# Kernel optimization log

Measured on AMD Instinct MI355X. Metric: run time of the kernel, lower is better.

The kernel has to match this reference:

```python
import jax, jax.numpy as jnp
import numpy as np

B = 128          # batch of codewords
M_CHK = 288      # n_check_nodes
N_VAR = 576      # n_variable_nodes
K_INFO = 288     # n_information_bits
N_ITER = 5
EDGE_P = 0.02    # ~11-12 edges per check row, LDPC-like sparsity


def setup_inputs() -> dict:
    key = jax.random.key(0)
    k1, k2, k3, k4 = jax.random.split(key, 4)
    inputs = jax.random.normal(k1, (B, N_VAR), dtype=jnp.float32)
    # sparse binary parity-check matrix, batched (keras RNN constants carry batch dim)
    H = jax.random.bernoulli(k2, EDGE_P, (B, M_CHK, N_VAR)).astype(jnp.float32)
    sigma2 = 0.5 + 0.5 * jax.random.uniform(k3, (B, 1), dtype=jnp.float32)
    # learned parameters
    input_ponderation = jnp.ones((N_ITER, 1), dtype=jnp.float32)
    out_ponderation = jnp.ones((N_ITER, 1), dtype=jnp.float32)
    skip_ponderation = jnp.ones((1, 1), dtype=jnp.float32)
    # per-edge check-to-variable weights of the neural BP cell
    w_cv = 1.0 + 0.02 * jax.random.normal(k4, (M_CHK, N_VAR), dtype=jnp.float32)
    gate_logit = jnp.asarray(0.0, dtype=jnp.float32)
    return {"inputs": inputs, "H": H, "sigma2": sigma2,
            "input_ponderation": input_ponderation,
            "out_ponderation": out_ponderation,
            "skip_ponderation": skip_ponderation,
            "w_cv": w_cv, "gate_logit": gate_logit}


def _decode(inputs, H, sigma2, input_ponderation, out_ponderation,
            skip_ponderation, w_cv, gate_logit):
    llrs = -4.0 * inputs / sigma2                                    # [B, n]
    # trainable=True path: normalize by mean |llr|
    norm_llrs = llrs / jnp.mean(jnp.abs(llrs), axis=-1, keepdims=True)
    # tile over iterations and apply input ponderation -> [B, T, n]
    x = norm_llrs[:, None, :] * input_ponderation

    mask = H                                                         # [B, m, n]
    gate = jax.nn.sigmoid(gate_logit)

    def cell(Mstate, x_t):
        # variable-to-check extrinsic messages on edges
        S = jnp.sum(Mstate, axis=1, keepdims=True)                   # [B, 1, n]
        V = (x_t[:, None, :] + S - Mstate) * mask                    # [B, m, n]
        # tanh-product check-node update (product excluding self via divide)
        t = jnp.tanh(0.5 * jnp.clip(V, -15.0, 15.0))
        t_edge = jnp.where(mask > 0, t, 1.0)
        P = jnp.prod(t_edge, axis=-1, keepdims=True)                 # [B, m, 1]
        t_safe = jnp.where(jnp.abs(t_edge) < 1e-7,
                           jnp.where(t_edge >= 0, 1e-7, -1e-7), t_edge)
        r = jnp.clip(P / t_safe, -1.0 + 1e-6, 1.0 - 1e-6)
        M_new = 2.0 * jnp.arctanh(r) * w_cv * mask                   # weighted c2v
        # gated (damped) state update
        M_out = gate * M_new + (1.0 - gate) * Mstate
        posterior = x_t + jnp.sum(M_out, axis=1)                     # [B, n]
        return M_out, posterior

    M0 = jnp.zeros_like(H)
    xs = jnp.swapaxes(x, 0, 1)                                       # [T, B, n]
    _, posts = jax.lax.scan(cell, M0, xs)
    outputs = jnp.swapaxes(posts, 0, 1)                              # [B, T, n]

    # post-normalization per iteration, weighted pooling over iterations
    norm_out = outputs / jnp.mean(jnp.abs(outputs), axis=-1, keepdims=True)
    pooled = jnp.mean(out_ponderation * norm_out, axis=-2)           # [B, n]
    out = pooled + skip_ponderation * norm_llrs                      # [1,1] broadcast
    return jax.nn.sigmoid(-out[:, :K_INFO])


def reference(inputs, H, sigma2, input_ponderation, out_ponderation,
              skip_ponderation, w_cv, gate_logit):
    return _decode(inputs, H, sigma2, input_ponderation, out_ponderation,
                   skip_ponderation, w_cv, gate_logit)
```

## Files before the change

kernel.cpp:

```cpp
#include <hip/hip_runtime.h>

#define B_SZ  128
#define MCHK  288
#define NVAR  576
#define KINFO 288
#define NITER 5
#define ECAP  3712
#define TPB   1024

__global__ __launch_bounds__(TPB) void decode(
    const float* __restrict__ inp,   const float* __restrict__ H,
    const float* __restrict__ sigma2,const float* __restrict__ ipond,
    const float* __restrict__ opond, const float* __restrict__ skipp,
    const float* __restrict__ wcv,   const float* __restrict__ gatel,
    float* __restrict__ out)
{
    __shared__ float Mld[ECAP];
    __shared__ float tld[ECAP];
    __shared__ float wld[ECAP];
    __shared__ unsigned int ev[ECAP];
    __shared__ float Sb[NITER + 1][NVAR];
    __shared__ float xln[NVAR];
    __shared__ float Prow[MCHK];
    __shared__ int   rcnt[MCHK], roff[MCHK];
    __shared__ float red[NITER * 16];
    __shared__ float scalv[NITER];
    __shared__ int   Ecnt;

    const int b    = blockIdx.x;
    const int tid  = threadIdx.x;
    const int wid  = tid >> 6;
    const int lane = tid & 63;

    const float sig  = sigma2[b];
    const float gate = 1.0f / (1.0f + __expf(-gatel[0]));
    const float gbar = 1.0f - gate;

    float ipl[NITER], opl[NITER];
    #pragma unroll
    for (int t = 0; t < NITER; ++t) { ipl[t] = ipond[t]; opl[t] = opond[t]; }

    float l = 0.0f, al = 0.0f, xv = 0.0f;
    if (tid < NVAR) { l = -4.0f * inp[(size_t)b * NVAR + tid] / sig; al = fabsf(l); }
    #pragma unroll
    for (int o = 32; o; o >>= 1) al += __shfl_down(al, o, 64);
    if (lane == 0) red[wid] = al;
    if (tid == 0) Ecnt = 0;
    for (int i = tid; i < (NITER + 1) * NVAR; i += TPB) ((float*)Sb)[i] = 0.0f;
    __syncthreads();
    if (wid == 0) {
        float s = (lane < 16) ? red[lane] : 0.0f;
        s += __shfl_down(s, 8, 64); s += __shfl_down(s, 4, 64);
        s += __shfl_down(s, 2, 64); s += __shfl_down(s, 1, 64);
        if (lane == 0) scalv[0] = (float)NVAR / s;
    }
    __syncthreads();
    if (tid < NVAR) { xv = l * scalv[0]; xln[tid] = xv; }

    {
        const float* Hb = H + (size_t)b * MCHK * NVAR;
        const unsigned long long lt = (1ull << lane) - 1ull;
        for (int i = 0; i < MCHK / 16; ++i) {
            int r = wid + 16 * i;
            const float4* h4 = (const float4*)(Hb + (size_t)r * NVAR);
            const float4* w4 = (const float4*)(wcv + (size_t)r * NVAR);
            float4 a  = h4[lane];
            float4 b4 = h4[64 + lane];
            float  c  = ((const float*)h4)[512 + lane];
            float4 wa = w4[lane];
            float4 wb = w4[64 + lane];
            float  wc = ((const float*)w4)[512 + lane];
            unsigned long long mk[9];
            mk[0]=__ballot(a.x!=0.f);  mk[1]=__ballot(a.y!=0.f);
            mk[2]=__ballot(a.z!=0.f);  mk[3]=__ballot(a.w!=0.f);
            mk[4]=__ballot(b4.x!=0.f); mk[5]=__ballot(b4.y!=0.f);
            mk[6]=__ballot(b4.z!=0.f); mk[7]=__ballot(b4.w!=0.f);
            mk[8]=__ballot(c!=0.f);
            int tot = 0;
            #pragma unroll
            for (int k = 0; k < 9; ++k) tot += __popcll(mk[k]);
            int o0 = 0;
            if (lane == 0) o0 = atomicAdd(&Ecnt, tot);
            o0 = __shfl(o0, 0, 64);
            int cc = (o0 >= ECAP) ? 0 : ((o0 + tot > ECAP) ? (ECAP - o0) : tot);
            if (lane == 0) { roff[r] = o0; rcnt[r] = cc; }
            float wv[9] = {wa.x, wa.y, wa.z, wa.w, wb.x, wb.y, wb.z, wb.w, wc};
            int base = 0;
            #pragma unroll
            for (int k = 0; k < 9; ++k) {
                bool nz = (mk[k] >> lane) & 1ull;
                int col = (k < 4) ? (4 * lane + k)
                        : (k < 8) ? (256 + 4 * lane + (k - 4))
                                  : (512 + lane);
                if (nz) {
                    int p = base + __popcll(mk[k] & lt);
                    if (p < cc) {
                        int e = o0 + p;
                        ev[e]  = ((unsigned)r << 16) | (unsigned)col;
                        wld[e] = wv[k];
                        Mld[e] = 0.0f;
                    }
                }
                base += __popcll(mk[k]);
            }
        }
    }
    __syncthreads();
    const int E = (Ecnt > ECAP) ? ECAP : Ecnt;

    for (int t = 0; t < NITER; ++t) {
        const float pt = ipl[t];
        const float* St = Sb[t];
        float*       Sn = Sb[t + 1];

        for (int e = tid; e < E; e += TPB) {
            int v   = (int)(ev[e] & 0xFFFFu);
            float V = fmaf(pt, xln[v], St[v]) - Mld[e];
            V = fminf(15.0f, fmaxf(-15.0f, V));
            float ex = __expf(V);
            float te = (ex - 1.0f) * __builtin_amdgcn_rcpf(ex + 1.0f);
            float x  = 0.5f * V, x2 = x * x;
            float tp = x * fmaf(x2, fmaf(x2, fmaf(x2, -0.05396825f, 0.13333333f),
                                         -0.33333333f), 1.0f);
            tld[e] = (fabsf(V) < 0.5f) ? tp : te;
        }
        __syncthreads();

        if (tid < MCHK) {
            int o = roff[tid], oe = o + rcnt[tid];
            float p0 = 1.0f, p1 = 1.0f, p2 = 1.0f, p3 = 1.0f;
            int j = o;
            for (; j + 4 <= oe; j += 4) {
                float t0 = tld[j], t1 = tld[j + 1], t2 = tld[j + 2], t3 = tld[j + 3];
                p0 *= t0; p1 *= t1; p2 *= t2; p3 *= t3;
            }
            for (; j < oe; ++j) p0 *= tld[j];
            Prow[tid] = (p0 * p1) * (p2 * p3);
        }
        __syncthreads();

        for (int e = tid; e < E; e += TPB) {
            unsigned pk = ev[e];
            int v = (int)(pk & 0xFFFFu);
            int r = (int)(pk >> 16);
            float tj = tld[e];
            float ts = (fabsf(tj) < 1e-7f) ? ((tj >= 0.0f) ? 1e-7f : -1e-7f) : tj;
            float rr = Prow[r] * __builtin_amdgcn_rcpf(ts);
            rr = fminf(1.0f - 1e-6f, fmaxf(-1.0f + 1e-6f, rr));
            float Mn = __logf((1.0f + rr) * __builtin_amdgcn_rcpf(1.0f - rr)) * wld[e];
            float Mo = fmaf(gate, Mn, gbar * Mld[e]);
            Mld[e] = Mo;
            atomicAdd(&Sn[v], Mo);
        }
        __syncthreads();
    }

    float ap[NITER] = {0, 0, 0, 0, 0};
    if (tid < NVAR) {
        #pragma unroll
        for (int t = 0; t < NITER; ++t)
            ap[t] = fabsf(fmaf(ipl[t], xv, Sb[t + 1][tid]));
    }
    #pragma unroll
    for (int o = 32; o; o >>= 1) {
        #pragma unroll
        for (int t = 0; t < NITER; ++t) ap[t] += __shfl_down(ap[t], o, 64);
    }
    if (lane == 0) {
        #pragma unroll
        for (int t = 0; t < NITER; ++t) red[t * 16 + wid] = ap[t];
    }
    __syncthreads();
    if (wid == 0) {
        #pragma unroll
        for (int t = 0; t < NITER; ++t) {
            float s = (lane < 16) ? red[t * 16 + lane] : 0.0f;
            s += __shfl_down(s, 8, 64); s += __shfl_down(s, 4, 64);
            s += __shfl_down(s, 2, 64); s += __shfl_down(s, 1, 64);
            if (lane == 0) scalv[t] = (float)NVAR / s;
        }
    }
    __syncthreads();
    if (tid < KINFO) {
        float acc = 0.0f;
        #pragma unroll
        for (int t = 0; t < NITER; ++t)
            acc += opl[t] * fmaf(ipl[t], xv, Sb[t + 1][tid]) * scalv[t];
        float o = acc * (1.0f / NITER) + skipp[0] * xv;
        out[(size_t)b * KINFO + tid] = 1.0f / (1.0f + __expf(o));
    }
}

extern "C" void kernel_launch(void* const* d_in, const int* in_sizes, int n_in,
                              void* d_out, int out_size, void* d_ws, size_t ws_size,
                              hipStream_t stream) {
    const float* inp    = (const float*)d_in[0];
    const float* H      = (const float*)d_in[1];
    const float* sigma2 = (const float*)d_in[2];
    const float* ipond  = (const float*)d_in[3];
    const float* opond  = (const float*)d_in[4];
    const float* skipp  = (const float*)d_in[5];
    const float* wcv    = (const float*)d_in[6];
    const float* gatel  = (const float*)d_in[7];
    float* out = (float*)d_out;

    decode<<<B_SZ, TPB, 0, stream>>>(inp, H, sigma2, ipond, opond, skipp,
                                     wcv, gatel, out);
}
```

Measured before the change: 182.0 us.

## Build sparse edge list via flat H scan and per-row prefix scan

```diff
diff --git a/kernel.cpp b/kernel.cpp
--- a/kernel.cpp
+++ b/kernel.cpp
@@ -6,7 +6,10 @@
 #define KINFO 288
 #define NITER 5
 #define ECAP  3712
+#define CAP2  32
 #define TPB   1024
+#define NQ4   (MCHK * NVAR / 4)
+#define Q4ROW (NVAR / 4)
 
 __global__ __launch_bounds__(TPB) void decode(
     const float* __restrict__ inp,   const float* __restrict__ H,
@@ -23,9 +26,10 @@
     __shared__ float xln[NVAR];
     __shared__ float Prow[MCHK];
     __shared__ int   rcnt[MCHK], roff[MCHK];
+    __shared__ unsigned short vpad[MCHK * CAP2];
     __shared__ float red[NITER * 16];
     __shared__ float scalv[NITER];
-    __shared__ int   Ecnt;
+    __shared__ int   wtot[8], wbase[8];
 
     const int b    = blockIdx.x;
     const int tid  = threadIdx.x;
@@ -45,7 +49,7 @@
     #pragma unroll
     for (int o = 32; o; o >>= 1) al += __shfl_down(al, o, 64);
     if (lane == 0) red[wid] = al;
-    if (tid == 0) Ecnt = 0;
+    if (tid < MCHK) rcnt[tid] = 0;
     for (int i = tid; i < (NITER + 1) * NVAR; i += TPB) ((float*)Sb)[i] = 0.0f;
     __syncthreads();
     if (wid == 0) {
@@ -58,55 +62,65 @@
     if (tid < NVAR) { xv = l * scalv[0]; xln[tid] = xv; }
 
     {
-        const float* Hb = H + (size_t)b * MCHK * NVAR;
-        const unsigned long long lt = (1ull << lane) - 1ull;
-        for (int i = 0; i < MCHK / 16; ++i) {
-            int r = wid + 16 * i;
-            const float4* h4 = (const float4*)(Hb + (size_t)r * NVAR);
-            const float4* w4 = (const float4*)(wcv + (size_t)r * NVAR);
-            float4 a  = h4[lane];
-            float4 b4 = h4[64 + lane];
-            float  c  = ((const float*)h4)[512 + lane];
-            float4 wa = w4[lane];
-            float4 wb = w4[64 + lane];
-            float  wc = ((const float*)w4)[512 + lane];
-            unsigned long long mk[9];
-            mk[0]=__ballot(a.x!=0.f);  mk[1]=__ballot(a.y!=0.f);
-            mk[2]=__ballot(a.z!=0.f);  mk[3]=__ballot(a.w!=0.f);
-            mk[4]=__ballot(b4.x!=0.f); mk[5]=__ballot(b4.y!=0.f);
-            mk[6]=__ballot(b4.z!=0.f); mk[7]=__ballot(b4.w!=0.f);
-            mk[8]=__ballot(c!=0.f);
-            int tot = 0;
-            #pragma unroll
-            for (int k = 0; k < 9; ++k) tot += __popcll(mk[k]);
-            int o0 = 0;
-            if (lane == 0) o0 = atomicAdd(&Ecnt, tot);
-            o0 = __shfl(o0, 0, 64);
-            int cc = (o0 >= ECAP) ? 0 : ((o0 + tot > ECAP) ? (ECAP - o0) : tot);
-            if (lane == 0) { roff[r] = o0; rcnt[r] = cc; }
-            float wv[9] = {wa.x, wa.y, wa.z, wa.w, wb.x, wb.y, wb.z, wb.w, wc};
-            int base = 0;
-            #pragma unroll
-            for (int k = 0; k < 9; ++k) {
-                bool nz = (mk[k] >> lane) & 1ull;
-                int col = (k < 4) ? (4 * lane + k)
-                        : (k < 8) ? (256 + 4 * lane + (k - 4))
-                                  : (512 + lane);
-                if (nz) {
-                    int p = base + __popcll(mk[k] & lt);
-                    if (p < cc) {
-                        int e = o0 + p;
-                        ev[e]  = ((unsigned)r << 16) | (unsigned)col;
-                        wld[e] = wv[k];
-                        Mld[e] = 0.0f;
-                    }
-                }
-                base += __popcll(mk[k]);
+        const float4* H4 = (const float4*)(H + (size_t)b * MCHK * NVAR);
+        for (int k = 0; k < (NQ4 + TPB - 1) / TPB; ++k) {
+            int q = tid + k * TPB;
+            if (q >= NQ4) break;
+            float4 hv = H4[q];
+            if (hv.x != 0.f || hv.y != 0.f || hv.z != 0.f || hv.w != 0.f) {
+                int r  = q / Q4ROW;
+                int c0 = (q - r * Q4ROW) * 4;
+                unsigned short* vp = vpad + r * CAP2;
+                if (hv.x != 0.f) { int j = atomicAdd(&rcnt[r], 1); if (j < CAP2) vp[j] = (unsigned short)(c0);     }
+                if (hv.y != 0.f) { int j = atomicAdd(&rcnt[r], 1); if (j < CAP2) vp[j] = (unsigned short)(c0 + 1); }
+                if (hv.z != 0.f) { int j = atomicAdd(&rcnt[r], 1); if (j < CAP2) vp[j] = (unsigned short)(c0 + 2); }
+                if (hv.w != 0.f) { int j = atomicAdd(&rcnt[r], 1); if (j < CAP2) vp[j] = (unsigned short)(c0 + 3); }
             }
         }
     }
     __syncthreads();
-    const int E = (Ecnt > ECAP) ? ECAP : Ecnt;
+
+    int cc = 0, incl = 0;
+    if (tid < 512) {
+        cc = (tid < MCHK) ? rcnt[tid] : 0;
+        if (cc > CAP2) cc = CAP2;
+        incl = cc;
+        #pragma unroll
+        for (int o = 1; o < 64; o <<= 1) {
+            int n = __shfl_up(incl, o, 64);
+            if (lane >= o) incl += n;
+        }
+        if (lane == 63) wtot[wid] = incl;
+    }
+    __syncthreads();
+    if (tid == 0) {
+        int s = 0;
+        #pragma unroll
+        for (int i = 0; i < 8; ++i) { wbase[i] = s; s += wtot[i]; }
+    }
+    __syncthreads();
+    if (tid < MCHK) {
+        int o = incl + wbase[wid] - cc;
+        int ce = cc;
+        if (o >= ECAP)           { o = 0; ce = 0; }
+        else if (o + ce > ECAP)  { ce = ECAP - o; }
+        roff[tid] = o; rcnt[tid] = ce;
+    }
+    const int Etot = wbase[7] + wtot[7];
+    const int E    = (Etot > ECAP) ? ECAP : Etot;
+    __syncthreads();
+
+    for (int s = tid; s < MCHK * CAP2; s += TPB) {
+        int r = s >> 5, j = s & (CAP2 - 1);
+        if (j < rcnt[r]) {
+            int e   = roff[r] + j;
+            int col = vpad[s];
+            ev[e]  = ((unsigned)r << 16) | (unsigned)col;
+            wld[e] = wcv[r * NVAR + col];
+            Mld[e] = 0.0f;
+        }
+    }
+    __syncthreads();
 
     for (int t = 0; t < NITER; ++t) {
         const float pt = ipl[t];
```

New measurement: 189.2 us. +4.0%, slower.
